# Kernel optimization log

Measured on AMD Instinct MI355X. Metric: run time of the kernel, lower is better.

## Reference

```python
import jax, jax.numpy as jnp
import numpy as np

D_STATE = 11
DT_RANK = 4
BN_EPS = 1e-5
RMS_EPS = 1e-5


def setup_inputs() -> dict:
    key = jax.random.key(0)
    ks = jax.random.split(key, 8)
    B, L, D = 8, 8192, 64
    x = jax.random.normal(ks[0], (B, L, D), dtype=jnp.float32)
    tconv_w = jax.random.normal(ks[1], (64, 1, 63), dtype=jnp.float32) * 0.1
    bn_gamma = jnp.ones((64,), jnp.float32)
    bn_beta = jnp.zeros((64,), jnp.float32)
    x_proj_weight = jax.random.normal(ks[2], (1, DT_RANK + 2 * D_STATE, 64), jnp.float32) * (64 ** -0.5)
    dt_projs_weight = jax.random.uniform(ks[3], (1, 64, DT_RANK), jnp.float32, -0.5, 0.5)
    # dt bias ~ inverse-softplus of dt in [1e-3, 1e-1]
    dt = jnp.exp(jax.random.uniform(ks[4], (1, 64), jnp.float32) * (np.log(0.1) - np.log(0.001)) + np.log(0.001))
    dt_projs_bias = dt + jnp.log(-jnp.expm1(-dt))
    A_logs = jnp.log(jnp.broadcast_to(jnp.arange(1, D_STATE + 1, dtype=jnp.float32), (64, D_STATE)))
    Ds = jnp.ones((64,), jnp.float32)
    rms_scale = jnp.ones((1, 64), jnp.float32)
    return {"x": x, "tconv_w": tconv_w, "bn_gamma": bn_gamma, "bn_beta": bn_beta,
            "x_proj_weight": x_proj_weight, "dt_projs_weight": dt_projs_weight,
            "dt_projs_bias": dt_projs_bias, "A_logs": A_logs, "Ds": Ds,
            "rms_scale": rms_scale}


def _silu(v):
    return v * jax.nn.sigmoid(v)


def reference(x, tconv_w, bn_gamma, bn_beta, x_proj_weight, dt_projs_weight,
              dt_projs_bias, A_logs, Ds, rms_scale):
    B, L, D = x.shape  # D == 64
    z = x
    xc = jnp.transpose(x, (0, 2, 1))  # (B, C, L)

    # depthwise conv1d, kernel 63, pad 31, no bias
    xc = jax.lax.conv_general_dilated(
        xc, tconv_w, window_strides=(1,), padding=[(31, 31)],
        feature_group_count=D, dimension_numbers=("NCH", "OIH", "NCH"))

    # BatchNorm1d (training-mode forward: batch stats, biased variance)
    mean = jnp.mean(xc, axis=(0, 2), keepdims=True)
    var = jnp.mean((xc - mean) ** 2, axis=(0, 2), keepdims=True)
    xc = (xc - mean) / jnp.sqrt(var + BN_EPS) * bn_gamma[None, :, None] + bn_beta[None, :, None]

    u = _silu(xc)  # (B, d_inner, L)

    # x_proj: (B,d,L) x (C,d) -> (B,C,L)
    x_dbl = jnp.einsum("bdl,cd->bcl", u, x_proj_weight[0])
    dts = x_dbl[:, :DT_RANK]                      # (B, r, L)
    Bs = x_dbl[:, DT_RANK:DT_RANK + D_STATE]      # (B, N, L)
    Cs = x_dbl[:, DT_RANK + D_STATE:]             # (B, N, L)

    dts = jnp.einsum("brl,dr->bdl", dts, dt_projs_weight[0])
    delta = jax.nn.softplus(dts + dt_projs_bias[0][None, :, None])  # (B,d,L)

    A = -jnp.exp(A_logs)  # (d, N)
    dA = jnp.exp(jnp.einsum("bdl,dn->lbdn", delta, A))      # (L,B,d,N)
    dBu = jnp.einsum("bdl,bnl->lbdn", delta * u, Bs)        # (L,B,d,N)

    def step(h, inp):
        dA_t, dBu_t = inp
        h = dA_t * h + dBu_t
        return h, h

    h0 = jnp.zeros((B, u.shape[1], D_STATE), dtype=u.dtype)
    _, hs = jax.lax.scan(step, h0, (dA, dBu))  # (L,B,d,N)

    y = jnp.einsum("lbdn,bnl->bdl", hs, Cs) + Ds[None, :, None] * u  # (B,d,L)

    y = jnp.transpose(y, (0, 2, 1))  # (B, L, d_inner)

    # RMSNorm
    ms = jnp.mean(y ** 2, axis=-1, keepdims=True)
    y = (rms_scale / jnp.sqrt(ms + RMS_EPS)) * y

    out = y * _silu(z)
    return out
```

## Files before the change

### kernel.cpp

```cpp
#include <hip/hip_runtime.h>
#include <hip/hip_bf16.h>
#include <math.h>

#define NB 8
#define LL 8192
#define DD 64
#define NS 11
#define NR 4
#define NC 512
#define LC (LL/NC)
#define CONV_LT 128
#define KW 63
#define PJ 64
#define NBKT 64
#define US 68
#define WS 72

__device__ __forceinline__ float sigmoidf_(float v){ return 1.f/(1.f+__expf(-v)); }

__global__ void k_zero(float* __restrict__ p){
  p[blockIdx.x*256 + threadIdx.x] = 0.f;
}

__global__ __launch_bounds__(512,4) void k_conv(const float* __restrict__ x,
                                              const float* __restrict__ w,
                                              float* __restrict__ xc,
                                              float* __restrict__ bn_acc){
  const int b  = blockIdx.x / (LL/CONV_LT);
  const int lt = blockIdx.x % (LL/CONV_LT);
  const int l0 = lt*CONV_LT;
  __shared__ float xt[(CONV_LT+62)*DD];
  __shared__ float rs[512], rq[512];
  const int t = threadIdx.x;
  for (int i=t; i<(CONV_LT+62)*DD; i+=512){
    int lrel = i/DD, d = i%DD;
    int lg = l0 - 31 + lrel;
    xt[i] = (lg>=0 && lg<LL) ? x[((size_t)b*LL+lg)*DD + d] : 0.f;
  }
  __syncthreads();
  const int d = t & 63;
  const int base = (t >> 6) * 16;
  float acc[16];
  #pragma unroll
  for (int j=0;j<16;j++) acc[j]=0.f;
  #pragma unroll 1
  for (int kb=0; kb<4; ++kb){
    float wv[16];
    #pragma unroll
    for (int kk=0;kk<16;kk++){
      int k = kb*16+kk;
      wv[kk] = (k<KW) ? w[d*KW+k] : 0.f;
    }
    float xw[31];
    #pragma unroll
    for (int i=0;i<31;i++) xw[i] = xt[(base+kb*16+i)*DD + d];
    #pragma unroll
    for (int j=0;j<16;j++){
      #pragma unroll
      for (int kk=0;kk<16;kk++){
        acc[j] = fmaf(wv[kk], xw[j+kk], acc[j]);
      }
    }
  }
  float lsum=0.f, lsq=0.f;
  #pragma unroll
  for (int j=0;j<16;j++){
    xc[((size_t)b*LL + l0+base+j)*DD + d] = acc[j];
    lsum += acc[j]; lsq = fmaf(acc[j],acc[j],lsq);
  }
  rs[t]=lsum; rq[t]=lsq;
  __syncthreads();
  if (t<64){
    float s=0.f, q=0.f;
    #pragma unroll
    for (int g=0; g<8; ++g){ s += rs[t+64*g]; q += rq[t+64*g]; }
    const int bkt = (blockIdx.x & (NBKT-1))*128;
    atomicAdd(&bn_acc[bkt+t],    s);
    atomicAdd(&bn_acc[bkt+64+t], q);
  }
}

__global__ __launch_bounds__(256,4) void k_proj(const float* __restrict__ xc,
                                              const float* __restrict__ bn_acc,
                                              const float* __restrict__ gamma,
                                              const float* __restrict__ beta,
                                              const float* __restrict__ xpw,
                                              const float* __restrict__ dtw,
                                              const float* __restrict__ dtb,
                                              const float* __restrict__ Alog,
                                              float* __restrict__ duo,
                                              float* __restrict__ bc,
                                              float* __restrict__ chunkst){
  const int b  = blockIdx.x / (LL/PJ);
  const int lt = blockIdx.x % (LL/PJ);
  const int l0 = lt*PJ;
  __shared__ float ul[PJ*US];
  __shared__ float bcl[PJ][24];
  __shared__ float wsh2[26*WS];
  __shared__ float xd[PJ*NR];
  __shared__ float dtwsh[64*NR];
  __shared__ float bnred[2][4][64];
  const int t = threadIdx.x;
  for (int i=t; i<26*64; i+=256){ int c=i>>6, dd=i&63; wsh2[c*WS+dd] = xpw[i]; }
  dtwsh[t] = dtw[t];
  const int d = t & 63, wv = t >> 6;
  {
    float ms=0.f, qs=0.f;
    #pragma unroll
    for (int k=wv*16; k<wv*16+16; ++k){
      ms += bn_acc[k*128 + d];
      qs += bn_acc[k*128 + 64 + d];
    }
    bnred[0][wv][d]=ms; bnred[1][wv][d]=qs;
  }
  __syncthreads();
  float msum = bnred[0][0][d]+bnred[0][1][d]+bnred[0][2][d]+bnred[0][3][d];
  float qsum = bnred[1][0][d]+bnred[1][1][d]+bnred[1][2][d]+bnred[1][3][d];
  const float inv_n = 1.f/((float)NB*(float)LL);
  float mean = msum*inv_n;
  float var  = qsum*inv_n - mean*mean;
  float sc = gamma[d] * rsqrtf(var + 1e-5f);
  float sh = beta[d] - mean*sc;
  float uu[16];
  #pragma unroll
  for (int j=0;j<16;j++){
    int lr = wv*16 + j;
    float v = xc[((size_t)b*LL + l0+lr)*DD + d];
    v = fmaf(v, sc, sh);
    float u_ = v * sigmoidf_(v);
    uu[j] = u_;
    ul[lr*US+d] = u_;
  }
  __syncthreads();
  {
    const int cp  = t & 15;
    const int lrb = t >> 4;
    if (cp < 13){
      float acc0[4] = {0.f,0.f,0.f,0.f};
      float acc1[4] = {0.f,0.f,0.f,0.f};
      #pragma unroll 2
      for (int dd4=0; dd4<16; ++dd4){
        float4 w0 = *reinterpret_cast<const float4*>(&wsh2[(2*cp  )*WS + dd4*4]);
        float4 w1 = *reinterpret_cast<const float4*>(&wsh2[(2*cp+1)*WS + dd4*4]);
        #pragma unroll
        for (int p=0;p<4;p++){
          float4 uv = *reinterpret_cast<const float4*>(&ul[(lrb*4+p)*US + dd4*4]);
          acc0[p] = fmaf(w0.x,uv.x, fmaf(w0.y,uv.y, fmaf(w0.z,uv.z, fmaf(w0.w,uv.w, acc0[p]))));
          acc1[p] = fmaf(w1.x,uv.x, fmaf(w1.y,uv.y, fmaf(w1.z,uv.z, fmaf(w1.w,uv.w, acc1[p]))));
        }
      }
      #pragma unroll
      for (int cc=0; cc<2; ++cc){
        int c = 2*cp+cc;
        #pragma unroll
        for (int p=0;p<4;p++){
          int lr = lrb*4+p;
          float v = cc ? acc1[p] : acc0[p];
          if (c < NR) xd[lr*NR+c] = v;
          else {
            int pos = c - NR;
            int slot = (pos < NS) ? pos : pos+1;
            bcl[lr][slot] = v;
            bc[((size_t)b*LL + l0+lr)*24 + slot] = v;
          }
        }
      }
    }
  }
  __syncthreads();
  {
    const float bias = dtb[d];
    const float dw0 = dtwsh[d*NR+0], dw1 = dtwsh[d*NR+1],
                dw2 = dtwsh[d*NR+2], dw3 = dtwsh[d*NR+3];
    float a0 = -__expf(Alog[d*NS]);
    bool fast = true;
    #pragma unroll
    for (int n=1;n<NS;n++){
      float an = -__expf(Alog[d*NS+n]);
      fast = fast && (fabsf(an - (float)(n+1)*a0) <= 1e-4f*(float)(n+1));
    }
    const int task = b*NC + lt*4 + wv;
    float h[12];
    #pragma unroll
    for (int n=0;n<12;n++) h[n]=0.f;
    float dsum=0.f;
    float de_prev=0.f, u_prev=0.f;
    #pragma unroll 4
    for (int l=0;l<LC;++l){
      int lr = wv*LC + l;
      float4 xv = *reinterpret_cast<const float4*>(&xd[lr*NR]);
      float s = fmaf(dw0,xv.x, fmaf(dw1,xv.y, fmaf(dw2,xv.z, fmaf(dw3,xv.w, bias))));
      float de = fmaxf(s,0.f) + __logf(1.f + __expf(-fabsf(s)));
      float u_ = uu[l];
      float du = de*u_;
      dsum += de;
      if ((l & 1)==0){ de_prev = de; u_prev = u_; }
      else {
        float4 st; st.x = de_prev; st.y = u_prev; st.z = de; st.w = u_;
        size_t ph = (size_t)b*(LL/2) + (size_t)(l0 + lr - 1)/2;
        *reinterpret_cast<float4*>(duo + (ph*DD + d)*4) = st;
      }
      float bca[12];
      const float4* q = reinterpret_cast<const float4*>(&bcl[lr][0]);
      *reinterpret_cast<float4*>(&bca[0]) = q[0];
      *reinterpret_cast<float4*>(&bca[4]) = q[1];
      *reinterpret_cast<float4*>(&bca[8]) = q[2];
      if (fast){
        float r = __expf(a0*de);
        float dA = 1.f;
        #pragma unroll
        for (int n=0;n<NS;n++){
          dA *= r;
          h[n] = fmaf(dA, h[n], du*bca[n]);
        }
      } else {
        #pragma unroll
        for (int n=0;n<NS;n++){
          float dA = __expf(-__expf(Alog[d*NS+n])*de);
          h[n] = fmaf(dA, h[n], du*bca[n]);
        }
      }
    }
    h[11] = dsum;
    float4* o = reinterpret_cast<float4*>(chunkst + ((size_t)task*64 + d)*12);
    o[0] = *reinterpret_cast<float4*>(&h[0]);
    o[1] = *reinterpret_cast<float4*>(&h[4]);
    o[2] = *reinterpret_cast<float4*>(&h[8]);
  }
}

__global__ __launch_bounds__(64) void k_scanMid(const float* __restrict__ chunkst,
                                                const float* __restrict__ Alog,
                                                float* __restrict__ hin){
  const int wid  = blockIdx.x;
  const int lane = threadIdx.x & 63;
  const int b = wid >> 6, d = wid & 63;
  const int c0 = lane*8;
  const size_t recbase = (((size_t)b*NC + c0)*64 + d)*12;
  float aAll[NS];
  #pragma unroll
  for (int n=0;n<NS;n++) aAll[n] = -expf(Alog[d*NS+n]);
  bool fast = true;
  #pragma unroll
  for (int n=1;n<NS;n++)
    fast = fast && (fabsf(aAll[n] - (float)(n+1)*aAll[0]) <= 1e-4f*(float)(n+1));
  float Aa[NS], Bb[NS];
  #pragma unroll
  for (int n=0;n<NS;n++){ Aa[n]=1.f; Bb[n]=0.f; }
  #pragma unroll
  for (int j=0;j<8;j++){
    float rec[12];
    const float4* q = reinterpret_cast<const float4*>(chunkst + recbase + (size_t)j*768);
    *reinterpret_cast<float4*>(&rec[0]) = q[0];
    *reinterpret_cast<float4*>(&rec[4]) = q[1];
    *reinterpret_cast<float4*>(&rec[8]) = q[2];
    float ds = rec[11];
    if (fast){
      float r = __expf(aAll[0]*ds);
      float dA = 1.f;
      #pragma unroll
      for (int n=0;n<NS;n++){
        dA *= r;
        Bb[n] = fmaf(dA, Bb[n], rec[n]);
        Aa[n] *= dA;
      }
    } else {
      #pragma unroll
      for (int n=0;n<NS;n++){
        float dA = __expf(aAll[n]*ds);
        Bb[n] = fmaf(dA, Bb[n], rec[n]);
        Aa[n] *= dA;
      }
    }
  }
  #pragma unroll
  for (int n=0;n<NS;n++){
    float A = Aa[n], Bv = Bb[n];
    #pragma unroll
    for (int off=1; off<64; off<<=1){
      float Ap=__shfl_up(A,off,64), Bp=__shfl_up(Bv,off,64);
      if (lane>=off){ Bv = fmaf(A,Bp,Bv); A*=Ap; }
    }
    float hs = __shfl_up(Bv,1,64);
    Bb[n] = (lane==0) ? 0.f : hs;
  }
  #pragma unroll
  for (int j=0;j<8;j++){
    float rec[12];
    const float4* q = reinterpret_cast<const float4*>(chunkst + recbase + (size_t)j*768);
    *reinterpret_cast<float4*>(&rec[0]) = q[0];
    *reinterpret_cast<float4*>(&rec[4]) = q[1];
    *reinterpret_cast<float4*>(&rec[8]) = q[2];
    float ds = rec[11];
    float outv[12];
    if (fast){
      float r = __expf(aAll[0]*ds);
      float dA = 1.f;
      #pragma unroll
      for (int n=0;n<NS;n++){
        outv[n] = Bb[n];
        dA *= r;
        Bb[n] = fmaf(dA, Bb[n], rec[n]);
      }
    } else {
      #pragma unroll
      for (int n=0;n<NS;n++){
        outv[n] = Bb[n];
        float dA = __expf(aAll[n]*ds);
        Bb[n] = fmaf(dA, Bb[n], rec[n]);
      }
    }
    outv[11] = 0.f;
    float4* o = reinterpret_cast<float4*>(hin + recbase + (size_t)j*768);
    o[0] = *reinterpret_cast<float4*>(&outv[0]);
    o[1] = *reinterpret_cast<float4*>(&outv[4]);
    o[2] = *reinterpret_cast<float4*>(&outv[8]);
  }
}

__global__ __launch_bounds__(256,4) void k_scanB(const float* __restrict__ duo,
                                               const float* __restrict__ bc,
                                               const float* __restrict__ Alog,
                                               const float* __restrict__ hin,
                                               const float* __restrict__ Dsv,
                                               const float* __restrict__ rmss,
                                               const float* __restrict__ x,
                                               float* __restrict__ out){
  const int task = blockIdx.x*4 + (threadIdx.x>>6);
  const int d = threadIdx.x & 63;
  const int b = task / NC, c = task % NC;
  float a0 = -expf(Alog[d*NS]);
  bool fast = true;
  #pragma unroll
  for (int n=1;n<NS;n++){
    float an = -expf(Alog[d*NS+n]);
    fast = fast && (fabsf(an - (float)(n+1)*a0) <= 1e-4f*(float)(n+1));
  }
  float h[12];
  {
    const float4* q = reinterpret_cast<const float4*>(hin + ((size_t)task*64 + d)*12);
    *reinterpret_cast<float4*>(&h[0]) = q[0];
    *reinterpret_cast<float4*>(&h[4]) = q[1];
    *reinterpret_cast<float4*>(&h[8]) = q[2];
  }
  const float Dd = Dsv[d];
  const float rsc = rmss[d];
  const int l0 = c*LC;
  #pragma unroll 2
  for (int l2=0; l2<LC; l2+=2){
    size_t ph = (size_t)b*(LL/2) + (size_t)(l0+l2)/2;
    float4 dq = *reinterpret_cast<const float4*>(duo + (ph*DD + d)*4);
    #pragma unroll
    for (int s=0; s<2; ++s){
      size_t p = (size_t)b*LL + l0 + l2 + s;
      float de = s ? dq.z : dq.x;
      float uu = s ? dq.w : dq.y;
      float du = de*uu;
      float bca[24];
      const float4* q = reinterpret_cast<const float4*>(bc + p*24);
      *reinterpret_cast<float4*>(&bca[0])  = q[0];
      *reinterpret_cast<float4*>(&bca[4])  = q[1];
      *reinterpret_cast<float4*>(&bca[8])  = q[2];
      *reinterpret_cast<float4*>(&bca[12]) = q[3];
      *reinterpret_cast<float4*>(&bca[16]) = q[4];
      *reinterpret_cast<float4*>(&bca[20]) = q[5];
      float y = Dd*uu;
      if (fast){
        float r = __expf(a0*de);
        float dA = 1.f;
        #pragma unroll
        for (int n=0;n<NS;n++){
          dA *= r;
          h[n] = fmaf(dA, h[n], du*bca[n]);
          y = fmaf(h[n], bca[12+n], y);
        }
      } else {
        #pragma unroll
        for (int n=0;n<NS;n++){
          float dA = __expf(-expf(Alog[d*NS+n])*de);
          h[n] = fmaf(dA, h[n], du*bca[n]);
          y = fmaf(h[n], bca[12+n], y);
        }
      }
      float ss = y*y;
      #pragma unroll
      for (int m=1;m<64;m<<=1) ss += __shfl_xor(ss, m, 64);
      float yn = rsc * rsqrtf(ss*(1.f/64.f) + 1e-5f) * y;
      float z = x[p*DD+d];
      out[p*DD+d] = yn * (z * sigmoidf_(z));
    }
  }
}

extern "C" void kernel_launch(void* const* d_in, const int* in_sizes, int n_in,
                              void* d_out, int out_size, void* d_ws, size_t ws_size,
                              hipStream_t stream) {
  const float* x     = (const float*)d_in[0];
  const float* w     = (const float*)d_in[1];
  const float* gamma = (const float*)d_in[2];
  const float* beta  = (const float*)d_in[3];
  const float* xpw   = (const float*)d_in[4];
  const float* dtw   = (const float*)d_in[5];
  const float* dtb   = (const float*)d_in[6];
  const float* Alog  = (const float*)d_in[7];
  const float* Dsv   = (const float*)d_in[8];
  const float* rmss  = (const float*)d_in[9];
  float* out = (float*)d_out;

  float* f = (float*)d_ws;
  const size_t n_xld = (size_t)NB*LL*DD;
  float* xc      = f;
  float* duo     = xc + n_xld;
  float* bc      = duo + 2*n_xld;
  float* chunkst = bc + (size_t)NB*LL*24;
  float* hin     = chunkst + (size_t)NB*NC*64*12;
  float* bn_acc  = hin + (size_t)NB*NC*64*12;

  k_zero   <<<NBKT*128/256, 256, 0, stream>>>(bn_acc);
  k_conv   <<<NB*(LL/CONV_LT), 512, 0, stream>>>(x, w, xc, bn_acc);
  k_proj   <<<NB*(LL/PJ), 256, 0, stream>>>(xc, bn_acc, gamma, beta, xpw, dtw, dtb, Alog, duo, bc, chunkst);
  k_scanMid<<<NB*DD, 64, 0, stream>>>(chunkst, Alog, hin);
  k_scanB  <<<(NB*NC)/4, 256, 0, stream>>>(duo, bc, Alog, hin, Dsv, rmss, x, out);
}
```

Measured before the change: 90.48 us.

## Store conv output, delta/u and B/C intermediates in fp16

Switches the intermediate buffers (conv output xc, the delta/u pairs, and the B/C projections) from fp32 to fp16 storage. The local scan in the proj kernel rounds its inputs the same way, so its chunk states stay consistent with what the final scan reloads. This roughly halves the global memory traffic between kernels in this bandwidth-bound pipeline. The cost is reduced precision in delta, u, B and C, which could push accuracy toward the tolerance limit.

```diff
diff --git a/kernel.cpp b/kernel.cpp
--- a/kernel.cpp
+++ b/kernel.cpp
@@ -1,5 +1,6 @@
 #include <hip/hip_runtime.h>
 #include <hip/hip_bf16.h>
+#include <hip/hip_fp16.h>
 #include <math.h>
 
 #define NB 8
@@ -17,6 +18,7 @@
 #define WS 72
 
 __device__ __forceinline__ float sigmoidf_(float v){ return 1.f/(1.f+__expf(-v)); }
+__device__ __forceinline__ float rnd16(float v){ return __half2float(__float2half_rn(v)); }
 
 __global__ void k_zero(float* __restrict__ p){
   p[blockIdx.x*256 + threadIdx.x] = 0.f;
@@ -24,7 +26,7 @@
 
 __global__ __launch_bounds__(512,4) void k_conv(const float* __restrict__ x,
                                               const float* __restrict__ w,
-                                              float* __restrict__ xc,
+                                              __half* __restrict__ xc,
                                               float* __restrict__ bn_acc){
   const int b  = blockIdx.x / (LL/CONV_LT);
   const int lt = blockIdx.x % (LL/CONV_LT);
@@ -65,7 +67,7 @@
   float lsum=0.f, lsq=0.f;
   #pragma unroll
   for (int j=0;j<16;j++){
-    xc[((size_t)b*LL + l0+base+j)*DD + d] = acc[j];
+    xc[((size_t)b*LL + l0+base+j)*DD + d] = __float2half_rn(acc[j]);
     lsum += acc[j]; lsq = fmaf(acc[j],acc[j],lsq);
   }
   rs[t]=lsum; rq[t]=lsq;
@@ -80,7 +82,7 @@
   }
 }
 
-__global__ __launch_bounds__(256,4) void k_proj(const float* __restrict__ xc,
+__global__ __launch_bounds__(256,4) void k_proj(const __half* __restrict__ xc,
                                               const float* __restrict__ bn_acc,
                                               const float* __restrict__ gamma,
                                               const float* __restrict__ beta,
@@ -88,8 +90,8 @@
                                               const float* __restrict__ dtw,
                                               const float* __restrict__ dtb,
                                               const float* __restrict__ Alog,
-                                              float* __restrict__ duo,
-                                              float* __restrict__ bc,
+                                              __half2* __restrict__ duo,
+                                              __half* __restrict__ bch,
                                               float* __restrict__ chunkst){
   const int b  = blockIdx.x / (LL/PJ);
   const int lt = blockIdx.x % (LL/PJ);
@@ -125,9 +127,9 @@
   #pragma unroll
   for (int j=0;j<16;j++){
     int lr = wv*16 + j;
-    float v = xc[((size_t)b*LL + l0+lr)*DD + d];
+    float v = __half2float(xc[((size_t)b*LL + l0+lr)*DD + d]);
     v = fmaf(v, sc, sh);
-    float u_ = v * sigmoidf_(v);
+    float u_ = rnd16(v * sigmoidf_(v));
     uu[j] = u_;
     ul[lr*US+d] = u_;
   }
@@ -160,8 +162,9 @@
           else {
             int pos = c - NR;
             int slot = (pos < NS) ? pos : pos+1;
-            bcl[lr][slot] = v;
-            bc[((size_t)b*LL + l0+lr)*24 + slot] = v;
+            float vr = rnd16(v);
+            bcl[lr][slot] = vr;
+            bch[((size_t)b*LL + l0+lr)*24 + slot] = __float2half_rn(v);
           }
         }
       }
@@ -184,22 +187,16 @@
     #pragma unroll
     for (int n=0;n<12;n++) h[n]=0.f;
     float dsum=0.f;
-    float de_prev=0.f, u_prev=0.f;
     #pragma unroll 4
     for (int l=0;l<LC;++l){
       int lr = wv*LC + l;
       float4 xv = *reinterpret_cast<const float4*>(&xd[lr*NR]);
       float s = fmaf(dw0,xv.x, fmaf(dw1,xv.y, fmaf(dw2,xv.z, fmaf(dw3,xv.w, bias))));
-      float de = fmaxf(s,0.f) + __logf(1.f + __expf(-fabsf(s)));
+      float de = rnd16(fmaxf(s,0.f) + __logf(1.f + __expf(-fabsf(s))));
       float u_ = uu[l];
       float du = de*u_;
       dsum += de;
-      if ((l & 1)==0){ de_prev = de; u_prev = u_; }
-      else {
-        float4 st; st.x = de_prev; st.y = u_prev; st.z = de; st.w = u_;
-        size_t ph = (size_t)b*(LL/2) + (size_t)(l0 + lr - 1)/2;
-        *reinterpret_cast<float4*>(duo + (ph*DD + d)*4) = st;
-      }
+      duo[((size_t)b*LL + l0+lr)*DD + d] = __floats2half2_rn(de, u_);
       float bca[12];
       const float4* q = reinterpret_cast<const float4*>(&bcl[lr][0]);
       *reinterpret_cast<float4*>(&bca[0]) = q[0];
@@ -318,8 +315,8 @@
   }
 }
 
-__global__ __launch_bounds__(256,4) void k_scanB(const float* __restrict__ duo,
-                                               const float* __restrict__ bc,
+__global__ __launch_bounds__(256,4) void k_scanB(const __half2* __restrict__ duo,
+                                               const __half* __restrict__ bch,
                                                const float* __restrict__ Alog,
                                                const float* __restrict__ hin,
                                                const float* __restrict__ Dsv,
@@ -347,48 +344,46 @@
   const float rsc = rmss[d];
   const int l0 = c*LC;
   #pragma unroll 2
-  for (int l2=0; l2<LC; l2+=2){
-    size_t ph = (size_t)b*(LL/2) + (size_t)(l0+l2)/2;
-    float4 dq = *reinterpret_cast<const float4*>(duo + (ph*DD + d)*4);
-    #pragma unroll
-    for (int s=0; s<2; ++s){
-      size_t p = (size_t)b*LL + l0 + l2 + s;
-      float de = s ? dq.z : dq.x;
-      float uu = s ? dq.w : dq.y;
-      float du = de*uu;
-      float bca[24];
-      const float4* q = reinterpret_cast<const float4*>(bc + p*24);
-      *reinterpret_cast<float4*>(&bca[0])  = q[0];
-      *reinterpret_cast<float4*>(&bca[4])  = q[1];
-      *reinterpret_cast<float4*>(&bca[8])  = q[2];
-      *reinterpret_cast<float4*>(&bca[12]) = q[3];
-      *reinterpret_cast<float4*>(&bca[16]) = q[4];
-      *reinterpret_cast<float4*>(&bca[20]) = q[5];
-      float y = Dd*uu;
-      if (fast){
-        float r = __expf(a0*de);
-        float dA = 1.f;
-        #pragma unroll
-        for (int n=0;n<NS;n++){
-          dA *= r;
-          h[n] = fmaf(dA, h[n], du*bca[n]);
-          y = fmaf(h[n], bca[12+n], y);
-        }
-      } else {
-        #pragma unroll
-        for (int n=0;n<NS;n++){
-          float dA = __expf(-expf(Alog[d*NS+n])*de);
-          h[n] = fmaf(dA, h[n], du*bca[n]);
-          y = fmaf(h[n], bca[12+n], y);
-        }
-      }
-      float ss = y*y;
-      #pragma unroll
-      for (int m=1;m<64;m<<=1) ss += __shfl_xor(ss, m, 64);
-      float yn = rsc * rsqrtf(ss*(1.f/64.f) + 1e-5f) * y;
-      float z = x[p*DD+d];
-      out[p*DD+d] = yn * (z * sigmoidf_(z));
-    }
+  for (int l=l0; l<l0+LC; ++l){
+    size_t p = (size_t)b*LL + l;
+    __half2 dv = duo[p*DD+d];
+    float de = __low2float(dv), uu = __high2float(dv);
+    float du = de*uu;
+    __half2 h2[12];
+    {
+      const float4* q = reinterpret_cast<const float4*>(bch + p*24);
+      *reinterpret_cast<float4*>(&h2[0]) = q[0];
+      *reinterpret_cast<float4*>(&h2[4]) = q[1];
+      *reinterpret_cast<float4*>(&h2[8]) = q[2];
+    }
+    float y = Dd*uu;
+    if (fast){
+      float r = __expf(a0*de);
+      float dA = 1.f;
+      #pragma unroll
+      for (int n=0;n<NS;n++){
+        dA *= r;
+        float bn = (n&1) ? __high2float(h2[n>>1]) : __low2float(h2[n>>1]);
+        float cn = (n&1) ? __high2float(h2[(12+n)>>1]) : __low2float(h2[(12+n)>>1]);
+        h[n] = fmaf(dA, h[n], du*bn);
+        y = fmaf(h[n], cn, y);
+      }
+    } else {
+      #pragma unroll
+      for (int n=0;n<NS;n++){
+        float dA = __expf(-expf(Alog[d*NS+n])*de);
+        float bn = (n&1) ? __high2float(h2[n>>1]) : __low2float(h2[n>>1]);
+        float cn = (n&1) ? __high2float(h2[(12+n)>>1]) : __low2float(h2[(12+n)>>1]);
+        h[n] = fmaf(dA, h[n], du*bn);
+        y = fmaf(h[n], cn, y);
+      }
+    }
+    float ss = y*y;
+    #pragma unroll
+    for (int m=1;m<64;m<<=1) ss += __shfl_xor(ss, m, 64);
+    float yn = rsc * rsqrtf(ss*(1.f/64.f) + 1e-5f) * y;
+    float z = x[p*DD+d];
+    out[p*DD+d] = yn * (z * sigmoidf_(z));
   }
 }
 
@@ -409,16 +404,16 @@
 
   float* f = (float*)d_ws;
   const size_t n_xld = (size_t)NB*LL*DD;
-  float* xc      = f;
-  float* duo     = xc + n_xld;
-  float* bc      = duo + 2*n_xld;
-  float* chunkst = bc + (size_t)NB*LL*24;
+  __half*  xc  = (__half*)f;
+  __half2* duo = (__half2*)(f + n_xld);
+  __half*  bch = (__half*)(f + n_xld + 2*n_xld);
+  float* chunkst = f + n_xld + 2*n_xld + (size_t)NB*LL*24;
   float* hin     = chunkst + (size_t)NB*NC*64*12;
   float* bn_acc  = hin + (size_t)NB*NC*64*12;
 
   k_zero   <<<NBKT*128/256, 256, 0, stream>>>(bn_acc);
   k_conv   <<<NB*(LL/CONV_LT), 512, 0, stream>>>(x, w, xc, bn_acc);
-  k_proj   <<<NB*(LL/PJ), 256, 0, stream>>>(xc, bn_acc, gamma, beta, xpw, dtw, dtb, Alog, duo, bc, chunkst);
+  k_proj   <<<NB*(LL/PJ), 256, 0, stream>>>(xc, bn_acc, gamma, beta, xpw, dtw, dtb, Alog, duo, bch, chunkst);
   k_scanMid<<<NB*DD, 64, 0, stream>>>(chunkst, Alog, hin);
-  k_scanB  <<<(NB*NC)/4, 256, 0, stream>>>(duo, bc, Alog, hin, Dsv, rmss, x, out);
-}
+  k_scanB  <<<(NB*NC)/4, 256, 0, stream>>>(duo, bch, Alog, hin, Dsv, rmss, x, out);
+}
```

Result: no change. 89.14 us (-1.5%).
